# Kernel tuning notes

Measured on AMD Instinct MI355X. Metric: run time of the kernel, lower is better.

The kernel has to match this reference:

```python
import jax, jax.numpy as jnp
import numpy as np

CHAN = 24
INNER = 64
GROUPS = 8
M = 5
LAM = 1e-4
MAX_ITER = 25
BETA = 1.0
EPS = 1e-5
B, HH, WW = 128, 32, 32


def conv2d(x, w, b=None):
    # NCHW, OIHW, 3x3 SAME conv (padding = kernel//2)
    y = jax.lax.conv_general_dilated(x, w, (1, 1), 'SAME',
                                     dimension_numbers=('NCHW', 'OIHW', 'NCHW'))
    if b is not None:
        y = y + b[None, :, None, None]
    return y


def group_norm(x, g, b):
    bsz, c, h, w = x.shape
    xg = x.reshape(bsz, GROUPS, c // GROUPS, h, w)
    mu = xg.mean(axis=(2, 3, 4), keepdims=True)
    var = xg.var(axis=(2, 3, 4), keepdims=True)
    xn = ((xg - mu) / jnp.sqrt(var + EPS)).reshape(bsz, c, h, w)
    return xn * g[None, :, None, None] + b[None, :, None, None]


def batch_norm(x, g, b):
    # training-mode batch statistics over (N, H, W)
    mu = x.mean(axis=(0, 2, 3), keepdims=True)
    var = x.var(axis=(0, 2, 3), keepdims=True)
    return (x - mu) / jnp.sqrt(var + EPS) * g[None, :, None, None] + b[None, :, None, None]


def resnet_f(p, z, x):
    c1w, g1g, g1b, c2w, g2g, g2b, g3g, g3b = p
    y = group_norm(jax.nn.relu(conv2d(z, c1w)), g1g, g1b)
    return group_norm(jax.nn.relu(z + group_norm(x + conv2d(y, c2w), g2g, g2b)), g3g, g3b)


def anderson(f, x0):
    # Anderson acceleration, fixed MAX_ITER iterations (no host-sync tol break).
    bsz = x0.shape[0]
    d = x0.size // bsz
    X = jnp.zeros((bsz, M, d), x0.dtype)
    Fm = jnp.zeros((bsz, M, d), x0.dtype)
    f0 = f(x0).reshape(bsz, -1)
    X = X.at[:, 0].set(x0.reshape(bsz, -1))
    Fm = Fm.at[:, 0].set(f0)
    X = X.at[:, 1].set(f0)
    Fm = Fm.at[:, 1].set(f(f0.reshape(x0.shape)).reshape(bsz, -1))
    for k in range(2, MAX_ITER):
        n = min(k, M)
        G = Fm[:, :n] - X[:, :n]                       # [b, n, d]
        Hm = jnp.zeros((bsz, n + 1, n + 1), x0.dtype)
        Hm = Hm.at[:, 0, 1:].set(1.0).at[:, 1:, 0].set(1.0)
        Hm = Hm.at[:, 1:, 1:].set(jnp.einsum('bnd,bmd->bnm', G, G)
                                  + LAM * jnp.eye(n, dtype=x0.dtype)[None])
        yv = jnp.zeros((bsz, n + 1, 1), x0.dtype).at[:, 0, 0].set(1.0)
        alpha = jnp.linalg.solve(Hm, yv)[:, 1:, 0]     # [b, n]
        xnew = (BETA * jnp.einsum('bn,bnd->bd', alpha, Fm[:, :n])
                + (1.0 - BETA) * jnp.einsum('bn,bnd->bd', alpha, X[:, :n]))
        X = X.at[:, k % M].set(xnew)
        Fm = Fm.at[:, k % M].set(f(xnew.reshape(x0.shape)).reshape(bsz, -1))
    return X[:, (MAX_ITER - 1) % M].reshape(x0.shape)


def setup_inputs() -> dict:
    key = jax.random.key(0)
    ks = jax.random.split(key, 8)
    inp = {
        'x': jax.random.normal(ks[0], (B, 3, HH, WW), jnp.float32),
        'pre_conv_w': jax.random.normal(ks[1], (CHAN, 3, 3, 3), jnp.float32) * 0.1,
        'pre_conv_b': jnp.zeros((CHAN,), jnp.float32),
        'pre_bn_g': jnp.ones((CHAN,), jnp.float32),
        'pre_bn_b': jnp.zeros((CHAN,), jnp.float32),
        'f_conv1_w': jax.random.normal(ks[2], (INNER, CHAN, 3, 3), jnp.float32) * 0.01,
        'gn1_g': jnp.ones((INNER,), jnp.float32),
        'gn1_b': jnp.zeros((INNER,), jnp.float32),
        'f_conv2_w': jax.random.normal(ks[3], (CHAN, INNER, 3, 3), jnp.float32) * 0.01,
        'gn2_g': jnp.ones((CHAN,), jnp.float32),
        'gn2_b': jnp.zeros((CHAN,), jnp.float32),
        'gn3_g': jnp.ones((CHAN,), jnp.float32),
        'gn3_b': jnp.zeros((CHAN,), jnp.float32),
        'post_bn_g': jnp.ones((CHAN,), jnp.float32),
        'post_bn_b': jnp.zeros((CHAN,), jnp.float32),
        'fc_w': jax.random.normal(ks[4], (10, CHAN * 4 * 4), jnp.float32) * 0.05,
        'fc_b': jnp.zeros((10,), jnp.float32),
    }
    return inp


def reference(x, pre_conv_w, pre_conv_b, pre_bn_g, pre_bn_b,
              f_conv1_w, gn1_g, gn1_b, f_conv2_w, gn2_g, gn2_b, gn3_g, gn3_b,
              post_bn_g, post_bn_b, fc_w, fc_b):
    # pre: conv + BatchNorm
    xp = batch_norm(conv2d(x, pre_conv_w, pre_conv_b), pre_bn_g, pre_bn_b)
    p = (f_conv1_w, gn1_g, gn1_b, f_conv2_w, gn2_g, gn2_b, gn3_g, gn3_b)
    # DEQ fixed-point solve (eval path: train=False returns the fixed point)
    z_star = anderson(lambda z: resnet_f(p, z, xp), jnp.zeros_like(xp))
    z = resnet_f(p, z_star, xp)
    # post: relu -> BN -> avgpool(8,8) -> flatten -> linear
    h = batch_norm(jax.nn.relu(z), post_bn_g, post_bn_b)
    bsz, c, hh, ww = h.shape
    pooled = h.reshape(bsz, c, hh // 8, 8, ww // 8, 8).mean(axis=(3, 5))  # [B,C,4,4]
    return pooled.reshape(bsz, -1) @ fc_w.T + fc_b
```

## Files before the change

kernel.cpp:

```cpp
#include <hip/hip_runtime.h>
#include <hip/hip_bf16.h>

typedef __hip_bfloat16 bf16;
typedef unsigned short ushortT;
typedef __attribute__((ext_vector_type(8))) short short8;
typedef __attribute__((ext_vector_type(4))) float f32x4;

#define BB 128
#define CHAN 24
#define INNER 64
#define HW 1024
#define DD (CHAN*HW)

constexpr size_t cBD = (size_t)BB*DD;
constexpr size_t cYB = (size_t)BB*INNER*HW;

__device__ __attribute__((aligned(16))) ushortT g_xp[cBD];
__device__ __attribute__((aligned(16))) ushortT g_X[5*cBD];
__device__ __attribute__((aligned(16))) ushortT g_F[5*cBD];
__device__ __attribute__((aligned(16))) ushortT g_G[5*cBD];
__device__ __attribute__((aligned(16))) ushortT g_yb[cYB];
__device__ __attribute__((aligned(16))) ushortT g_tb[cBD];
__device__ __attribute__((aligned(16))) ushortT g_w1m[9*64*32];
__device__ __attribute__((aligned(16))) ushortT g_w2m[9*24*64];
__device__ __attribute__((aligned(16))) float g_stats2a[48];
__device__ __attribute__((aligned(16))) float g_stats2b[48];
__device__ __attribute__((aligned(16))) float g_gn1sum[BB*8*2];
__device__ __attribute__((aligned(16))) float g_gn2sum[BB*24*2];
__device__ __attribute__((aligned(16))) float g_gram[BB*25];
__device__ __attribute__((aligned(16))) float g_params[5120];
__device__ unsigned g_isbf16;

#define P_PCW 0
#define P_PCB 648
#define P_PBG 672
#define P_PBB 696
#define P_G1G 720
#define P_G1B 784
#define P_G2G 848
#define P_G2B 872
#define P_G3G 896
#define P_G3B 920
#define P_POG 944
#define P_POB 968
#define P_FCW 992
#define P_FCB 4832

__device__ __forceinline__ size_t aidx(int b, int icv, int pix){
  return (((size_t)b*3 + icv)*1024 + (size_t)pix)*8;
}
__device__ __forceinline__ float rdin(const void* p, int i){
  if (g_isbf16) return __bfloat162float(((const bf16*)p)[i]);
  return ((const float*)p)[i];
}
__device__ __forceinline__ float b2f(ushortT u){
  unsigned v = ((unsigned)u) << 16;
  return __builtin_bit_cast(float, v);
}
__device__ __forceinline__ ushortT f2b(float f){
  unsigned u = __builtin_bit_cast(unsigned, f);
  u += 0x7FFFu + ((u >> 16) & 1u);
  return (ushortT)(u >> 16);
}
__device__ __forceinline__ void ld24c(const ushortT* base, int b, int pix, float* o){
  #pragma unroll
  for (int icv=0;icv<3;icv++){
    short8 v = *(const short8*)&base[aidx(b,icv,pix)];
    #pragma unroll
    for (int j=0;j<8;j++) o[icv*8+j] = b2f((ushortT)v[j]);
  }
}
__device__ __forceinline__ void st24c(ushortT* base, int b, int pix, const float* i){
  #pragma unroll
  for (int icv=0;icv<3;icv++){
    short8 v;
    #pragma unroll
    for (int j=0;j<8;j++) v[j] = (short)f2b(i[icv*8+j]);
    *(short8*)&base[aidx(b,icv,pix)] = v;
  }
}

__global__ void detect_k(const void* g1g){
  if (threadIdx.x==0 && blockIdx.x==0){
    unsigned u = *(const unsigned*)g1g;
    g_isbf16 = (u == 0x3F803F80u) ? 1u : 0u;
  }
}

__global__ void cvt_params_k(const void* pcw, const void* pcb, const void* pbg, const void* pbb,
                             const void* g1g, const void* g1b, const void* g2g, const void* g2b,
                             const void* g3g, const void* g3b, const void* pog, const void* pob,
                             const void* fcw, const void* fcb){
  int t = threadIdx.x;
  for (int i=t;i<648;i+=256)  g_params[P_PCW+i]=rdin(pcw,i);
  for (int i=t;i<24;i+=256) { g_params[P_PCB+i]=rdin(pcb,i);
                              g_params[P_PBG+i]=rdin(pbg,i);
                              g_params[P_PBB+i]=rdin(pbb,i);
                              g_params[P_G2G+i]=rdin(g2g,i);
                              g_params[P_G2B+i]=rdin(g2b,i);
                              g_params[P_G3G+i]=rdin(g3g,i);
                              g_params[P_G3B+i]=rdin(g3b,i);
                              g_params[P_POG+i]=rdin(pog,i);
                              g_params[P_POB+i]=rdin(pob,i); }
  for (int i=t;i<64;i+=256) { g_params[P_G1G+i]=rdin(g1g,i);
                              g_params[P_G1B+i]=rdin(g1b,i); }
  for (int i=t;i<3840;i+=256) g_params[P_FCW+i]=rdin(fcw,i);
  for (int i=t;i<10;i+=256)   g_params[P_FCB+i]=rdin(fcb,i);
  for (int i=t;i<48;i+=256) { g_stats2a[i]=0.f; g_stats2b[i]=0.f; }
}

__global__ void wtm_k(const void* w1, const void* w2){
  int t = blockIdx.x*256 + threadIdx.x;
  if (t < 9*64*32){
    int ic = t & 31, oc = (t>>5)&63, s9 = t>>11;
    float v = (ic<24) ? rdin(w1, (oc*24+ic)*9 + s9) : 0.f;
    g_w1m[t] = f2b(v);
  }
  int u = t - 9*64*32;
  if (u >= 0 && u < 9*24*64){
    int ic = u & 63; int rest = u >> 6; int oc = rest % 24; int s9 = rest / 24;
    g_w2m[u] = f2b(rdin(w2, (oc*64+ic)*9 + s9));
  }
}

__global__ void zero0_k(){
  size_t base = ((size_t)blockIdx.x*256 + threadIdx.x)*8;
  short8 z = {0,0,0,0,0,0,0,0};
  *(short8*)&g_yb[base] = z;
  if (blockIdx.x < 1536) *(short8*)&g_X[base] = z;
  int t = blockIdx.x*256 + threadIdx.x;
  if (blockIdx.x < 8)  g_gn1sum[t] = 0.f;
  if (blockIdx.x < 24) g_gn2sum[t] = 0.f;
}

__global__ void preconv_k(const void* __restrict__ x){
  __shared__ float sR2d[4*48];
  int id = blockIdx.x*256 + threadIdx.x;
  int b = id >> 10, pix = id & 1023;
  int yy = pix >> 5, xx = pix & 31;
  float acc[24];
  #pragma unroll
  for (int oc=0;oc<24;oc++) acc[oc] = g_params[P_PCB+oc];
  for (int ic=0; ic<3; ic++)
    for (int ky=0; ky<3; ky++){
      int gy = yy+ky-1; if (gy<0||gy>=32) continue;
      for (int kx=0;kx<3;kx++){
        int gx = xx+kx-1; if (gx<0||gx>=32) continue;
        float v = rdin(x, ((b*3+ic)*32+gy)*32+gx);
        #pragma unroll
        for (int oc=0;oc<24;oc++)
          acc[oc] += v * g_params[P_PCW+(oc*3+ic)*9+ky*3+kx];
      }
    }
  st24c(g_tb, b, pix, acc);
  int lane = threadIdx.x & 63, wv = threadIdx.x >> 6;
  #pragma unroll
  for (int c=0;c<24;c++){
    float r = acc[c], q = acc[c]*acc[c];
    #pragma unroll
    for (int off=32;off;off>>=1){ r += __shfl_down(r,off,64); q += __shfl_down(q,off,64); }
    if (lane==0){ sR2d[wv*48+c*2]=r; sR2d[wv*48+c*2+1]=q; }
  }
  __syncthreads();
  if (threadIdx.x < 48)
    atomicAdd(&g_stats2a[threadIdx.x],
      sR2d[threadIdx.x] + sR2d[48+threadIdx.x] + sR2d[96+threadIdx.x] + sR2d[144+threadIdx.x]);
}

__global__ void bn_apply_k(){
  int id = blockIdx.x*256+threadIdx.x;
  int b = id >> 10, pix = id & 1023;
  const float inv = 1.f/(BB*HW);
  float tv[24], ov[24];
  ld24c(g_tb, b, pix, tv);
  #pragma unroll
  for (int c=0;c<24;c++){
    float mean = g_stats2a[c*2]*inv;
    float var = fmaxf(g_stats2a[c*2+1]*inv - mean*mean, 0.f);
    float rstd = rsqrtf(var + 1e-5f);
    ov[c] = (tv[c]-mean)*rstd*g_params[P_PBG+c] + g_params[P_PBB+c];
  }
  st24c(g_xp, b, pix, ov);
}

__launch_bounds__(256, 2)
__global__ void conv1_k(int s){
  __shared__ ushortT sMem[29312];
  ushortT* sA = sMem;
  ushortT* sW = sMem + 10880;
  const int tid = threadIdx.x;
  const int lane = tid & 63, wv = tid >> 6;
  const int mLane = lane & 15, q = lane >> 4;
  const int b = blockIdx.x >> 2, yt = blockIdx.x & 3;
  const ushortT* __restrict__ Xs = g_X + (size_t)s*cBD;
  if (blockIdx.x < 24) g_gn2sum[blockIdx.x*256 + tid] = 0.f;
  for (int i = tid; i < 1360; i += 256){
    int icv = i & 3, apix = i >> 2;
    int yl = apix / 34, xl = apix - yl*34;
    int gy = yt*8 - 1 + yl, gx = xl - 1;
    short8 v = {0,0,0,0,0,0,0,0};
    if (gy >= 0 && gy < 32 && gx >= 0 && gx < 32 && icv < 3)
      v = *(const short8*)&Xs[aidx(b, icv, gy*32 + gx)];
    *(short8*)&sA[(size_t)(apix*4 + (icv ^ (apix&3)))*8] = v;
  }
  for (int i = tid; i < 2304; i += 256){
    int icv = i & 3, rest = i >> 2;
    int oc = rest & 63, s9 = rest >> 6;
    short8 v = *(const short8*)&g_w1m[(size_t)((s9*64 + oc)*32) + icv*8];
    *(short8*)&sW[(size_t)((s9*64+oc)*4 + (icv ^ (oc&3)))*8] = v;
  }
  __syncthreads();
  f32x4 acc[4][4];
  #pragma unroll
  for (int mt=0;mt<4;mt++)
    #pragma unroll
    for (int nt=0;nt<4;nt++) acc[mt][nt] = (f32x4){0.f,0.f,0.f,0.f};
  for (int s9=0; s9<9; s9++){
    int ky = s9/3, kx = s9 - ky*3;
    short8 bfr[4];
    #pragma unroll
    for (int nt=0;nt<4;nt++){
      int oc = nt*16 + mLane;
      bfr[nt] = *(const short8*)&sW[(size_t)((s9*64+oc)*4 + (q ^ (oc&3)))*8];
    }
    #pragma unroll
    for (int mt=0;mt<4;mt++){
      int g = wv*4+mt;
      int apix = ((g>>1) + ky)*34 + (g&1)*16 + mLane + kx;
      short8 afr = *(const short8*)&sA[(size_t)(apix*4 + (q ^ (apix&3)))*8];
      #pragma unroll
      for (int nt=0;nt<4;nt++)
        acc[mt][nt] = __builtin_amdgcn_mfma_f32_16x16x32_bf16(afr, bfr[nt], acc[mt][nt], 0,0,0);
    }
  }
  __syncthreads();
  ushortT* sOut = sMem;
  #pragma unroll
  for (int mt=0;mt<4;mt++){
    int g = wv*4+mt;
    #pragma unroll
    for (int nt=0;nt<4;nt++){
      int oc = nt*16 + mLane;
      #pragma unroll
      for (int r=0;r<4;r++){
        int pix = (g>>1)*32 + (g&1)*16 + q*4 + r;
        sOut[pix*64 + oc] = f2b(fmaxf(acc[mt][nt][r], 0.f));
      }
    }
  }
  __syncthreads();
  float s0=0.f, s1=0.f;
  size_t gbase = ((size_t)b*1024 + yt*256)*64;
  for (int c = tid; c < 2048; c += 256){
    short8 v = *(const short8*)&sOut[c*8];
    *(short8*)&g_yb[gbase + (size_t)c*8] = v;
    #pragma unroll
    for (int j=0;j<8;j++){ float f = b2f((ushortT)v[j]); s0 += f; s1 += f*f; }
  }
  s0 += __shfl_down(s0,32); s1 += __shfl_down(s1,32);
  s0 += __shfl_down(s0,16); s1 += __shfl_down(s1,16);
  s0 += __shfl_down(s0, 8); s1 += __shfl_down(s1, 8);
  if (lane < 8){
    atomicAdd(&g_gn1sum[(b*8+lane)*2],   s0);
    atomicAdd(&g_gn1sum[(b*8+lane)*2+1], s1);
  }
}

__launch_bounds__(256, 2)
__global__ void conv2_k(){
  __shared__ ushortT sMem[35584];
  __shared__ float sAff[128];
  ushortT* sA = sMem;
  ushortT* sW = sMem + 21760;
  const int tid = threadIdx.x;
  const int lane = tid & 63, wv = tid >> 6;
  const int mLane = lane & 15, q = lane >> 4;
  const int b = blockIdx.x >> 2, yt = blockIdx.x & 3;
  if (tid < 64){
    int c = tid, gr = c>>3;
    float S = g_gn1sum[(b*8+gr)*2], Q = g_gn1sum[(b*8+gr)*2+1];
    float mean = S*(1.f/8192.f);
    float var = fmaxf(Q*(1.f/8192.f) - mean*mean, 0.f);
    float rstd = rsqrtf(var + 1e-5f);
    float sc = rstd*g_params[P_G1G+c];
    sAff[c] = sc; sAff[64+c] = g_params[P_G1B+c] - mean*sc;
  }
  __syncthreads();
  for (int i = tid; i < 2720; i += 256){
    int icv = i & 7, apix = i >> 3;
    int yl = apix / 34, xl = apix - yl*34;
    int gy = yt*8 - 1 + yl, gx = xl - 1;
    short8 v = {0,0,0,0,0,0,0,0};
    if (gy >= 0 && gy < 32 && gx >= 0 && gx < 32){
      short8 raw = *(const short8*)&g_yb[((size_t)b*1024 + gy*32+gx)*64 + icv*8];
      #pragma unroll
      for (int j=0;j<8;j++){
        int c = icv*8+j;
        v[j] = (short)f2b(b2f((ushortT)raw[j])*sAff[c] + sAff[64+c]);
      }
    }
    *(short8*)&sA[(size_t)(apix*8 + (icv ^ (apix&7)))*8] = v;
  }
  for (int i = tid; i < 1728; i += 256){
    int icv = i & 7, rest = i >> 3;
    int oc = rest % 24, s9 = rest / 24;
    short8 v = *(const short8*)&g_w2m[(size_t)((s9*24+oc)*64) + icv*8];
    *(short8*)&sW[(size_t)((s9*24+oc)*8 + (icv ^ (oc&7)))*8] = v;
  }
  __syncthreads();
  f32x4 acc[4][2];
  #pragma unroll
  for (int mt=0;mt<4;mt++){ acc[mt][0]=(f32x4){0.f,0.f,0.f,0.f}; acc[mt][1]=(f32x4){0.f,0.f,0.f,0.f}; }
  const bool nt1ok = (mLane < 8);
  for (int s9=0; s9<9; s9++){
    int ky = s9/3, kx = s9 - ky*3;
    #pragma unroll
    for (int ks=0; ks<2; ks++){
      int ib = ks*4;
      short8 bfr[2];
      { int oc = mLane;
        bfr[0] = *(const short8*)&sW[(size_t)((s9*24+oc)*8 + ((ib+q) ^ (oc&7)))*8]; }
      if (nt1ok){
        int oc = 16 + mLane;
        bfr[1] = *(const short8*)&sW[(size_t)((s9*24+oc)*8 + ((ib+q) ^ (oc&7)))*8];
      } else bfr[1] = (short8){0,0,0,0,0,0,0,0};
      #pragma unroll
      for (int mt=0;mt<4;mt++){
        int g = wv*4+mt;
        int apix = ((g>>1) + ky)*34 + (g&1)*16 + mLane + kx;
        short8 afr = *(const short8*)&sA[(size_t)(apix*8 + ((ib+q) ^ (apix&7)))*8];
        acc[mt][0] = __builtin_amdgcn_mfma_f32_16x16x32_bf16(afr, bfr[0], acc[mt][0], 0,0,0);
        acc[mt][1] = __builtin_amdgcn_mfma_f32_16x16x32_bf16(afr, bfr[1], acc[mt][1], 0,0,0);
      }
    }
  }
  #pragma unroll
  for (int nt=0;nt<2;nt++){
    int oc = nt*16 + mLane;
    bool ok = (oc < 24);
    int icv = oc >> 3, e = oc & 7;
    float s0=0.f, s1=0.f;
    if (ok){
      #pragma unroll
      for (int mt=0;mt<4;mt++){
        int g = wv*4+mt;
        #pragma unroll
        for (int r=0;r<4;r++){
          int pix = (yt*8 + (g>>1))*32 + (g&1)*16 + q*4 + r;
          size_t o = aidx(b, icv, pix) + e;
          float v = acc[mt][nt][r] + b2f(g_xp[o]);
          g_tb[o] = f2b(v);
          s0 += v; s1 += v*v;
        }
      }
    }
    s0 += __shfl_down(s0,32); s1 += __shfl_down(s1,32);
    s0 += __shfl_down(s0,16); s1 += __shfl_down(s1,16);
    if (lane < 16 && ok){
      atomicAdd(&g_gn2sum[(b*24+oc)*2],   s0);
      atomicAdd(&g_gn2sum[(b*24+oc)*2+1], s1);
    }
  }
}

template<int N>
__device__ __forceinline__ void chol_alpha(const float Kf[5][5], float* alpha){
  double K[N][N];
  #pragma unroll
  for (int i=0;i<N;i++)
    #pragma unroll
    for (int j=0;j<N;j++)
      K[i][j] = (double)Kf[i][j] + (i==j ? 1e-4 : 0.0);
  #pragma unroll
  for (int c=0;c<N;c++){
    double d = K[c][c];
    #pragma unroll
    for (int k2=0;k2<c;k2++) d -= K[c][k2]*K[c][k2];
    d = sqrt(fmax(d, 1e-300));
    K[c][c] = d;
    double inv = 1.0/d;
    #pragma unroll
    for (int r=c+1;r<N;r++){
      double v = K[r][c];
      #pragma unroll
      for (int k2=0;k2<c;k2++) v -= K[r][k2]*K[c][k2];
      K[r][c] = v*inv;
    }
  }
  double y[N];
  #pragma unroll
  for (int i=0;i<N;i++){
    double v = 1.0;
    #pragma unroll
    for (int j=0;j<i;j++) v -= K[i][j]*y[j];
    y[i] = v / K[i][i];
  }
  double w[N];
  #pragma unroll
  for (int i=N-1;i>=0;i--){
    double v = y[i];
    #pragma unroll
    for (int j=i+1;j<N;j++) v -= K[j][i]*w[j];
    w[i] = v / K[i][i];
  }
  double sum = 0.0;
  #pragma unroll
  for (int i=0;i<N;i++) sum += w[i];
  double invs = 1.0/sum;
  #pragma unroll
  for (int i=0;i<N;i++) alpha[i] = (float)(w[i]*invs);
}

__launch_bounds__(1024)
__global__ void fuse_k(int s, int n, int snext){
  __shared__ float sM2[8], sR2[8], sM3[8], sR3[8];
  __shared__ float sSc2[24], sSb2[24], sSc3[24], sSb3[24];
  __shared__ float sRed[16*16];
  __shared__ float sRedG[16*5];
  __shared__ float sAlpha[5];
  __shared__ float sStat[16*48];
  const int b = blockIdx.x;
  const int t = threadIdx.x;
  const int lane = t & 63, wv = t >> 6;
  if (t < 16) g_gn1sum[b*16 + t] = 0.f;
  if (t < 8){
    float S = g_gn2sum[(b*24+t*3)*2]   + g_gn2sum[(b*24+t*3+1)*2]   + g_gn2sum[(b*24+t*3+2)*2];
    float Q = g_gn2sum[(b*24+t*3)*2+1] + g_gn2sum[(b*24+t*3+1)*2+1] + g_gn2sum[(b*24+t*3+2)*2+1];
    float m = S*(1.f/3072.f);
    sM2[t] = m;
    sR2[t] = rsqrtf(fmaxf(Q*(1.f/3072.f) - m*m, 0.f) + 1e-5f);
  }
  __syncthreads();
  if (t < 24){
    int g = t/3;
    float sc = sR2[g]*g_params[P_G2G+t];
    sSc2[t] = sc; sSb2[t] = g_params[P_G2B+t] - sM2[g]*sc;
  }
  __syncthreads();
  float xv[24], v[24];
  ld24c(g_tb, b, t, v);
  ld24c(g_X + (size_t)s*cBD, b, t, xv);
  float p0[8], p1[8];
  #pragma unroll
  for (int g=0;g<8;g++){ p0[g]=0.f; p1[g]=0.f; }
  #pragma unroll
  for (int c=0;c<24;c++){
    float val = fmaxf(xv[c] + v[c]*sSc2[c] + sSb2[c], 0.f);
    v[c] = val;
    int g = c/3;
    p0[g] += val; p1[g] += val*val;
  }
  #pragma unroll
  for (int g=0;g<8;g++){
    #pragma unroll
    for (int off=32;off;off>>=1){ p0[g]+=__shfl_down(p0[g],off,64); p1[g]+=__shfl_down(p1[g],off,64); }
  }
  if (lane==0){
    #pragma unroll
    for (int g=0;g<8;g++){ sRed[wv*16+g*2]=p0[g]; sRed[wv*16+g*2+1]=p1[g]; }
  }
  __syncthreads();
  if (t < 8){
    float S=0.f, Q=0.f;
    #pragma unroll
    for (int w=0;w<16;w++){ S += sRed[w*16+t*2]; Q += sRed[w*16+t*2+1]; }
    float m = S*(1.f/3072.f);
    sM3[t] = m;
    sR3[t] = rsqrtf(fmaxf(Q*(1.f/3072.f) - m*m, 0.f) + 1e-5f);
  }
  __syncthreads();
  if (t < 24){
    int g = t/3;
    float sc = sR3[g]*g_params[P_G3G+t];
    sSc3[t] = sc; sSb3[t] = g_params[P_G3B+t] - sM3[g]*sc;
  }
  __syncthreads();
  float fv[24];
  #pragma unroll
  for (int c=0;c<24;c++) fv[c] = v[c]*sSc3[c] + sSb3[c];
  st24c(g_F + (size_t)s*cBD, b, t, fv);

  if (n > 0){
    float gl[24];
    #pragma unroll
    for (int c=0;c<24;c++) gl[c] = b2f(f2b(fv[c] - xv[c]));
    st24c(g_G + (size_t)s*cBD, b, t, gl);
    float part[5];
    #pragma unroll
    for (int j=0;j<5;j++) part[j] = 0.f;
    #pragma unroll
    for (int j=0;j<5;j++){
      if (j >= n) continue;
      float acc = 0.f;
      if (j == s){
        #pragma unroll
        for (int c=0;c<24;c++) acc += gl[c]*gl[c];
      } else {
        float gv[24];
        ld24c(g_G + (size_t)j*cBD, b, t, gv);
        #pragma unroll
        for (int c=0;c<24;c++) acc += gl[c]*gv[c];
      }
      part[j] = acc;
    }
    #pragma unroll
    for (int j=0;j<5;j++){
      float vv = part[j];
      #pragma unroll
      for (int off=32;off;off>>=1) vv += __shfl_down(vv,off,64);
      if (lane==0) sRedG[wv*5+j] = vv;
    }
    __syncthreads();
    if (t == 0){
      for (int j=0;j<n;j++){
        float vv = 0.f;
        for (int w=0;w<16;w++) vv += sRedG[w*5+j];
        g_gram[b*25+s*5+j] = vv;
        g_gram[b*25+j*5+s] = vv;
      }
      float Kf[5][5];
      for (int i=0;i<n;i++)
        for (int j=0;j<n;j++) Kf[i][j] = g_gram[b*25+i*5+j];
      float al[5];
      if (n==1) al[0]=1.f;
      else if (n==2) chol_alpha<2>(Kf, al);
      else if (n==3) chol_alpha<3>(Kf, al);
      else if (n==4) chol_alpha<4>(Kf, al);
      else chol_alpha<5>(Kf, al);
      for (int j=0;j<n;j++) sAlpha[j] = al[j];
    }
    __syncthreads();
    float acc[24];
    #pragma unroll
    for (int c=0;c<24;c++) acc[c] = 0.f;
    #pragma unroll
    for (int j=0;j<5;j++){
      if (j >= n) continue;
      float aj = sAlpha[j];
      if (j == s){
        #pragma unroll
        for (int c=0;c<24;c++) acc[c] += aj*b2f(f2b(fv[c]));
      } else {
        float tv2[24];
        ld24c(g_F + (size_t)j*cBD, b, t, tv2);
        #pragma unroll
        for (int c=0;c<24;c++) acc[c] += aj*tv2[c];
      }
    }
    st24c(g_X + (size_t)snext*cBD, b, t, acc);
  } else {
    #pragma unroll
    for (int c=0;c<24;c++){
      float r = fmaxf(b2f(f2b(fv[c])), 0.f);
      float q = r*r;
      #pragma unroll
      for (int off=32;off;off>>=1){ r += __shfl_down(r,off,64); q += __shfl_down(q,off,64); }
      if (lane==0){ sStat[wv*48+c*2]=r; sStat[wv*48+c*2+1]=q; }
    }
    __syncthreads();
    if (t < 48){
      float vv = 0.f;
      #pragma unroll
      for (int w=0;w<16;w++) vv += sStat[w*48+t];
      atomicAdd(&g_stats2b[t], vv);
    }
  }
}

__global__ void postfc_k(void* __restrict__ out){
  __shared__ float sPool[384];
  __shared__ float sMean[24], sRstd[24];
  int b = blockIdx.x, t = threadIdx.x;
  if (t < 24){
    const float inv = 1.f/(BB*HW);
    float mean = g_stats2b[t*2]*inv;
    float var = fmaxf(g_stats2b[t*2+1]*inv - mean*mean, 0.f);
    sMean[t] = mean; sRstd[t] = rsqrtf(var + 1e-5f);
  }
  __syncthreads();
  const ushortT* z = g_F + 4*cBD;
  for (int i=t; i<384; i+=256){
    int c = i>>4, bin = i&15, ph = bin>>2, pw = bin&3;
    int icv = c>>3, e = c&7;
    float gg = g_params[P_POG+c], bv = g_params[P_POB+c];
    float mean = sMean[c], rstd = sRstd[c];
    float sum = 0.f;
    for (int dy=0;dy<8;dy++)
      for (int dx=0;dx<8;dx++){
        int pix = (ph*8+dy)*32 + pw*8+dx;
        float vv = fmaxf(b2f(z[aidx(b,icv,pix) + e]), 0.f);
        sum += (vv-mean)*rstd*gg + bv;
      }
    sPool[i] = sum*(1.f/64.f);
  }
  __syncthreads();
  if (t < 10){
    float s2 = g_params[P_FCB+t];
    for (int k2=0;k2<384;k2++) s2 += sPool[k2]*g_params[P_FCW+t*384+k2];
    if (g_isbf16) ((bf16*)out)[b*10+t] = __float2bfloat16(s2);
    else ((float*)out)[b*10+t] = s2;
  }
}

extern "C" void kernel_launch(void* const* d_in, const int* in_sizes, int n_in,
                              void* d_out, int out_size, void* d_ws, size_t ws_size,
                              hipStream_t stream){
  const void* x   = d_in[0];
  const void* pcw = d_in[1];
  const void* pcb = d_in[2];
  const void* pbg = d_in[3];
  const void* pbb = d_in[4];
  const void* w1  = d_in[5];
  const void* g1g = d_in[6];
  const void* g1b = d_in[7];
  const void* w2  = d_in[8];
  const void* g2g = d_in[9];
  const void* g2b = d_in[10];
  const void* g3g = d_in[11];
  const void* g3b = d_in[12];
  const void* pog = d_in[13];
  const void* pob = d_in[14];
  const void* fcw = d_in[15];
  const void* fcb = d_in[16];
  (void)d_ws; (void)ws_size; (void)in_sizes; (void)n_in; (void)out_size;

  detect_k<<<1,64,0,stream>>>(g1g);
  cvt_params_k<<<1,256,0,stream>>>(pcw,pcb,pbg,pbb,g1g,g1b,g2g,g2b,g3g,g3b,pog,pob,fcw,fcb);
  wtm_k<<<126,256,0,stream>>>(w1, w2);

  preconv_k<<<512,256,0,stream>>>(x);
  bn_apply_k<<<512,256,0,stream>>>();

  zero0_k<<<4096,256,0,stream>>>();
  conv2_k<<<512,256,0,stream>>>();
  fuse_k<<<128,1024,0,stream>>>(0, 1, 1);

  for (int k=1;k<25;k++){
    int s = k%5;
    conv1_k<<<512,256,0,stream>>>(s);
    conv2_k<<<512,256,0,stream>>>();
    if (k < 24){
      int n = (k+1 < 5) ? (k+1) : 5;
      fuse_k<<<128,1024,0,stream>>>(s, n, (k+1)%5);
    } else {
      fuse_k<<<128,1024,0,stream>>>(s, 0, -1);
    }
  }

  postfc_k<<<128,256,0,stream>>>(d_out);
}
```

Baseline: 1.452 ms.

## Split fuse kernel into two 512-block passes and fold Anderson mixing into conv1

```diff
diff --git a/kernel.cpp b/kernel.cpp
--- a/kernel.cpp
+++ b/kernel.cpp
@@ -4,6 +4,7 @@
 typedef __hip_bfloat16 bf16;
 typedef unsigned short ushortT;
 typedef __attribute__((ext_vector_type(8))) short short8;
+typedef __attribute__((ext_vector_type(4))) short s16x4;
 typedef __attribute__((ext_vector_type(4))) float f32x4;
 
 #define BB 128
@@ -16,7 +17,7 @@
 constexpr size_t cYB = (size_t)BB*INNER*HW;
 
 __device__ __attribute__((aligned(16))) ushortT g_xp[cBD];
-__device__ __attribute__((aligned(16))) ushortT g_X[5*cBD];
+__device__ __attribute__((aligned(16))) ushortT g_xcur[cBD];
 __device__ __attribute__((aligned(16))) ushortT g_F[5*cBD];
 __device__ __attribute__((aligned(16))) ushortT g_G[5*cBD];
 __device__ __attribute__((aligned(16))) ushortT g_yb[cYB];
@@ -27,6 +28,8 @@
 __device__ __attribute__((aligned(16))) float g_stats2b[48];
 __device__ __attribute__((aligned(16))) float g_gn1sum[BB*8*2];
 __device__ __attribute__((aligned(16))) float g_gn2sum[BB*24*2];
+__device__ __attribute__((aligned(16))) float g_gn3p[BB*4*16];
+__device__ __attribute__((aligned(16))) float g_gramp[BB*4*5*5];
 __device__ __attribute__((aligned(16))) float g_gram[BB*25];
 __device__ __attribute__((aligned(16))) float g_params[5120];
 __device__ unsigned g_isbf16;
@@ -48,6 +51,9 @@
 
 __device__ __forceinline__ size_t aidx(int b, int icv, int pix){
   return (((size_t)b*3 + icv)*1024 + (size_t)pix)*8;
+}
+__device__ __forceinline__ size_t tidx(int b, int g, int c, int p){
+  return ((((size_t)b*64 + g)*24 + c)<<4) + p;
 }
 __device__ __forceinline__ float rdin(const void* p, int i){
   if (g_isbf16) return __bfloat162float(((const bf16*)p)[i]);
@@ -127,10 +133,9 @@
   size_t base = ((size_t)blockIdx.x*256 + threadIdx.x)*8;
   short8 z = {0,0,0,0,0,0,0,0};
   *(short8*)&g_yb[base] = z;
-  if (blockIdx.x < 1536) *(short8*)&g_X[base] = z;
-  int t = blockIdx.x*256 + threadIdx.x;
-  if (blockIdx.x < 8)  g_gn1sum[t] = 0.f;
-  if (blockIdx.x < 24) g_gn2sum[t] = 0.f;
+  if (blockIdx.x < 1536) *(short8*)&g_xcur[base] = z;
+  if (blockIdx.x < 8)  g_gn1sum[blockIdx.x*256 + threadIdx.x] = 0.f;
+  if (blockIdx.x >= 8 && blockIdx.x < 32) g_gn2sum[(blockIdx.x-8)*256 + threadIdx.x] = 0.f;
 }
 
 __global__ void preconv_k(const void* __restrict__ x){
@@ -171,36 +176,122 @@
   int id = blockIdx.x*256+threadIdx.x;
   int b = id >> 10, pix = id & 1023;
   const float inv = 1.f/(BB*HW);
-  float tv[24], ov[24];
+  float tv[24];
   ld24c(g_tb, b, pix, tv);
+  int g = pix >> 4, p = pix & 15;
   #pragma unroll
   for (int c=0;c<24;c++){
     float mean = g_stats2a[c*2]*inv;
     float var = fmaxf(g_stats2a[c*2+1]*inv - mean*mean, 0.f);
     float rstd = rsqrtf(var + 1e-5f);
-    ov[c] = (tv[c]-mean)*rstd*g_params[P_PBG+c] + g_params[P_PBB+c];
-  }
-  st24c(g_xp, b, pix, ov);
+    float ov = (tv[c]-mean)*rstd*g_params[P_PBG+c] + g_params[P_PBB+c];
+    g_xp[tidx(b,g,c,p)] = f2b(ov);
+  }
+}
+
+template<int N>
+__device__ __forceinline__ void chol_alpha(const float Kf[5][5], float* alpha){
+  double K[N][N];
+  #pragma unroll
+  for (int i=0;i<N;i++)
+    #pragma unroll
+    for (int j=0;j<N;j++)
+      K[i][j] = (double)Kf[i][j] + (i==j ? 1e-4 : 0.0);
+  #pragma unroll
+  for (int c=0;c<N;c++){
+    double d = K[c][c];
+    #pragma unroll
+    for (int k2=0;k2<c;k2++) d -= K[c][k2]*K[c][k2];
+    d = sqrt(fmax(d, 1e-300));
+    K[c][c] = d;
+    double inv = 1.0/d;
+    #pragma unroll
+    for (int r=c+1;r<N;r++){
+      double v = K[r][c];
+      #pragma unroll
+      for (int k2=0;k2<c;k2++) v -= K[r][k2]*K[c][k2];
+      K[r][c] = v*inv;
+    }
+  }
+  double y[N];
+  #pragma unroll
+  for (int i=0;i<N;i++){
+    double v = 1.0;
+    #pragma unroll
+    for (int j=0;j<i;j++) v -= K[i][j]*y[j];
+    y[i] = v / K[i][i];
+  }
+  double w[N];
+  #pragma unroll
+  for (int i=N-1;i>=0;i--){
+    double v = y[i];
+    #pragma unroll
+    for (int j=i+1;j<N;j++) v -= K[j][i]*w[j];
+    w[i] = v / K[i][i];
+  }
+  double sum = 0.0;
+  #pragma unroll
+  for (int i=0;i<N;i++) sum += w[i];
+  double invs = 1.0/sum;
+  #pragma unroll
+  for (int i=0;i<N;i++) alpha[i] = (float)(w[i]*invs);
 }
 
 __launch_bounds__(256, 2)
-__global__ void conv1_k(int s){
+__global__ void conv1_k(int na, int rA){
   __shared__ ushortT sMem[29312];
+  __shared__ float sAlpha[5];
   ushortT* sA = sMem;
   ushortT* sW = sMem + 10880;
   const int tid = threadIdx.x;
   const int lane = tid & 63, wv = tid >> 6;
   const int mLane = lane & 15, q = lane >> 4;
   const int b = blockIdx.x >> 2, yt = blockIdx.x & 3;
-  const ushortT* __restrict__ Xs = g_X + (size_t)s*cBD;
   if (blockIdx.x < 24) g_gn2sum[blockIdx.x*256 + tid] = 0.f;
+  if (tid == 0){
+    float Kf[5][5];
+    for (int i=0;i<na;i++)
+      for (int j=0;j<na;j++) Kf[i][j] = g_gram[b*25 + i*5 + j];
+    for (int j=0;j<na;j++){
+      float v = g_gramp[((b*4+0)*5 + rA)*5 + j] + g_gramp[((b*4+1)*5 + rA)*5 + j]
+              + g_gramp[((b*4+2)*5 + rA)*5 + j] + g_gramp[((b*4+3)*5 + rA)*5 + j];
+      Kf[rA][j] = v; Kf[j][rA] = v;
+    }
+    if (yt == 0)
+      for (int j=0;j<na;j++){ g_gram[b*25+rA*5+j]=Kf[rA][j]; g_gram[b*25+j*5+rA]=Kf[rA][j]; }
+    float al[5];
+    if (na==1) al[0]=1.f;
+    else if (na==2) chol_alpha<2>(Kf, al);
+    else if (na==3) chol_alpha<3>(Kf, al);
+    else if (na==4) chol_alpha<4>(Kf, al);
+    else chol_alpha<5>(Kf, al);
+    for (int j=0;j<na;j++) sAlpha[j] = al[j];
+  }
+  __syncthreads();
+  float al[5];
+  #pragma unroll
+  for (int j=0;j<5;j++) al[j] = (j<na) ? sAlpha[j] : 0.f;
   for (int i = tid; i < 1360; i += 256){
     int icv = i & 3, apix = i >> 2;
     int yl = apix / 34, xl = apix - yl*34;
     int gy = yt*8 - 1 + yl, gx = xl - 1;
     short8 v = {0,0,0,0,0,0,0,0};
-    if (gy >= 0 && gy < 32 && gx >= 0 && gx < 32 && icv < 3)
-      v = *(const short8*)&Xs[aidx(b, icv, gy*32 + gx)];
+    if (gy >= 0 && gy < 32 && gx >= 0 && gx < 32 && icv < 3){
+      int pix = gy*32 + gx;
+      float acc[8] = {0.f,0.f,0.f,0.f,0.f,0.f,0.f,0.f};
+      #pragma unroll
+      for (int j=0;j<5;j++){
+        if (j < na){
+          short8 f = *(const short8*)&g_F[(size_t)j*cBD + aidx(b,icv,pix)];
+          #pragma unroll
+          for (int e=0;e<8;e++) acc[e] += al[j]*b2f((ushortT)f[e]);
+        }
+      }
+      #pragma unroll
+      for (int e=0;e<8;e++) v[e] = (short)f2b(acc[e]);
+      if (yl >= 1 && yl < 9 && xl >= 1 && xl < 33)
+        *(short8*)&g_xcur[aidx(b,icv,pix)] = v;
+    }
     *(short8*)&sA[(size_t)(apix*4 + (icv ^ (apix&3)))*8] = v;
   }
   for (int i = tid; i < 2304; i += 256){
@@ -344,11 +435,13 @@
       #pragma unroll
       for (int mt=0;mt<4;mt++){
         int g = wv*4+mt;
+        int grp = (yt*8 + (g>>1))*2 + (g&1);
+        s16x4 xpv = *(const s16x4*)&g_xp[tidx(b, grp, oc, q*4)];
         #pragma unroll
         for (int r=0;r<4;r++){
           int pix = (yt*8 + (g>>1))*32 + (g&1)*16 + q*4 + r;
           size_t o = aidx(b, icv, pix) + e;
-          float v = acc[mt][nt][r] + b2f(g_xp[o]);
+          float v = acc[mt][nt][r] + b2f((ushortT)xpv[r]);
           g_tb[o] = f2b(v);
           s0 += v; s1 += v*v;
         }
@@ -363,66 +456,13 @@
   }
 }
 
-template<int N>
-__device__ __forceinline__ void chol_alpha(const float Kf[5][5], float* alpha){
-  double K[N][N];
-  #pragma unroll
-  for (int i=0;i<N;i++)
-    #pragma unroll
-    for (int j=0;j<N;j++)
-      K[i][j] = (double)Kf[i][j] + (i==j ? 1e-4 : 0.0);
-  #pragma unroll
-  for (int c=0;c<N;c++){
-    double d = K[c][c];
-    #pragma unroll
-    for (int k2=0;k2<c;k2++) d -= K[c][k2]*K[c][k2];
-    d = sqrt(fmax(d, 1e-300));
-    K[c][c] = d;
-    double inv = 1.0/d;
-    #pragma unroll
-    for (int r=c+1;r<N;r++){
-      double v = K[r][c];
-      #pragma unroll
-      for (int k2=0;k2<c;k2++) v -= K[r][k2]*K[c][k2];
-      K[r][c] = v*inv;
-    }
-  }
-  double y[N];
-  #pragma unroll
-  for (int i=0;i<N;i++){
-    double v = 1.0;
-    #pragma unroll
-    for (int j=0;j<i;j++) v -= K[i][j]*y[j];
-    y[i] = v / K[i][i];
-  }
-  double w[N];
-  #pragma unroll
-  for (int i=N-1;i>=0;i--){
-    double v = y[i];
-    #pragma unroll
-    for (int j=i+1;j<N;j++) v -= K[j][i]*w[j];
-    w[i] = v / K[i][i];
-  }
-  double sum = 0.0;
-  #pragma unroll
-  for (int i=0;i<N;i++) sum += w[i];
-  double invs = 1.0/sum;
-  #pragma unroll
-  for (int i=0;i<N;i++) alpha[i] = (float)(w[i]*invs);
-}
-
-__launch_bounds__(1024)
-__global__ void fuse_k(int s, int n, int snext){
-  __shared__ float sM2[8], sR2[8], sM3[8], sR3[8];
-  __shared__ float sSc2[24], sSb2[24], sSc3[24], sSb3[24];
-  __shared__ float sRed[16*16];
-  __shared__ float sRedG[16*5];
-  __shared__ float sAlpha[5];
-  __shared__ float sStat[16*48];
-  const int b = blockIdx.x;
+__launch_bounds__(256)
+__global__ void fuse_a_k(){
+  __shared__ float sM2[8], sR2[8], sSc2[24], sSb2[24];
+  __shared__ float sRed[64];
+  const int b = blockIdx.x>>2, seg = blockIdx.x&3;
   const int t = threadIdx.x;
-  const int lane = t & 63, wv = t >> 6;
-  if (t < 16) g_gn1sum[b*16 + t] = 0.f;
+  if (seg == 0 && t < 16) g_gn1sum[b*16 + t] = 0.f;
   if (t < 8){
     float S = g_gn2sum[(b*24+t*3)*2]   + g_gn2sum[(b*24+t*3+1)*2]   + g_gn2sum[(b*24+t*3+2)*2];
     float Q = g_gn2sum[(b*24+t*3)*2+1] + g_gn2sum[(b*24+t*3+1)*2+1] + g_gn2sum[(b*24+t*3+2)*2+1];
@@ -437,133 +477,124 @@
     sSc2[t] = sc; sSb2[t] = g_params[P_G2B+t] - sM2[g]*sc;
   }
   __syncthreads();
-  float xv[24], v[24];
-  ld24c(g_tb, b, t, v);
-  ld24c(g_X + (size_t)s*cBD, b, t, xv);
+  const int pix = seg*256 + t;
+  float tv[24], xv[24];
+  ld24c(g_tb, b, pix, tv);
+  ld24c(g_xcur, b, pix, xv);
   float p0[8], p1[8];
   #pragma unroll
   for (int g=0;g<8;g++){ p0[g]=0.f; p1[g]=0.f; }
   #pragma unroll
   for (int c=0;c<24;c++){
-    float val = fmaxf(xv[c] + v[c]*sSc2[c] + sSb2[c], 0.f);
-    v[c] = val;
     int g = c/3;
-    p0[g] += val; p1[g] += val*val;
+    float v = fmaxf(xv[c] + tv[c]*sSc2[c] + sSb2[c], 0.f);
+    p0[g] += v; p1[g] += v*v;
   }
   #pragma unroll
   for (int g=0;g<8;g++){
-    #pragma unroll
-    for (int off=32;off;off>>=1){ p0[g]+=__shfl_down(p0[g],off,64); p1[g]+=__shfl_down(p1[g],off,64); }
-  }
+    for (int off=32;off>0;off>>=1){ p0[g]+=__shfl_down(p0[g],off,64); p1[g]+=__shfl_down(p1[g],off,64); }
+  }
+  int lane = t&63, wv = t>>6;
   if (lane==0){
     #pragma unroll
     for (int g=0;g<8;g++){ sRed[wv*16+g*2]=p0[g]; sRed[wv*16+g*2+1]=p1[g]; }
   }
   __syncthreads();
+  if (t < 16){
+    g_gn3p[(b*4+seg)*16 + t] = sRed[t]+sRed[16+t]+sRed[32+t]+sRed[48+t];
+  }
+}
+
+__launch_bounds__(256)
+__global__ void fuse_b_k(int s, int nv){
+  __shared__ float sM2[8], sR2[8], sM3[8], sR3[8];
+  __shared__ float sSc2[24], sSb2[24], sSc3[24], sSb3[24];
+  __shared__ float sRedG[4][5];
+  __shared__ float sR2d[4*48];
+  const int b = blockIdx.x>>2, seg = blockIdx.x&3;
+  const int t = threadIdx.x;
   if (t < 8){
-    float S=0.f, Q=0.f;
-    #pragma unroll
-    for (int w=0;w<16;w++){ S += sRed[w*16+t*2]; Q += sRed[w*16+t*2+1]; }
+    float S = g_gn2sum[(b*24+t*3)*2]   + g_gn2sum[(b*24+t*3+1)*2]   + g_gn2sum[(b*24+t*3+2)*2];
+    float Q = g_gn2sum[(b*24+t*3)*2+1] + g_gn2sum[(b*24+t*3+1)*2+1] + g_gn2sum[(b*24+t*3+2)*2+1];
     float m = S*(1.f/3072.f);
-    sM3[t] = m;
-    sR3[t] = rsqrtf(fmaxf(Q*(1.f/3072.f) - m*m, 0.f) + 1e-5f);
+    sM2[t] = m;
+    sR2[t] = rsqrtf(fmaxf(Q*(1.f/3072.f) - m*m, 0.f) + 1e-5f);
+    float S3 = g_gn3p[(b*4+0)*16+t*2]   + g_gn3p[(b*4+1)*16+t*2]
+             + g_gn3p[(b*4+2)*16+t*2]   + g_gn3p[(b*4+3)*16+t*2];
+    float Q3 = g_gn3p[(b*4+0)*16+t*2+1] + g_gn3p[(b*4+1)*16+t*2+1]
+             + g_gn3p[(b*4+2)*16+t*2+1] + g_gn3p[(b*4+3)*16+t*2+1];
+    float m3 = S3*(1.f/3072.f);
+    sM3[t] = m3;
+    sR3[t] = rsqrtf(fmaxf(Q3*(1.f/3072.f) - m3*m3, 0.f) + 1e-5f);
   }
   __syncthreads();
   if (t < 24){
     int g = t/3;
-    float sc = sR3[g]*g_params[P_G3G+t];
-    sSc3[t] = sc; sSb3[t] = g_params[P_G3B+t] - sM3[g]*sc;
-  }
-  __syncthreads();
-  float fv[24];
-  #pragma unroll
-  for (int c=0;c<24;c++) fv[c] = v[c]*sSc3[c] + sSb3[c];
-  st24c(g_F + (size_t)s*cBD, b, t, fv);
-
-  if (n > 0){
-    float gl[24];
-    #pragma unroll
-    for (int c=0;c<24;c++) gl[c] = b2f(f2b(fv[c] - xv[c]));
-    st24c(g_G + (size_t)s*cBD, b, t, gl);
-    float part[5];
-    #pragma unroll
-    for (int j=0;j<5;j++) part[j] = 0.f;
-    #pragma unroll
-    for (int j=0;j<5;j++){
-      if (j >= n) continue;
-      float acc = 0.f;
-      if (j == s){
-        #pragma unroll
-        for (int c=0;c<24;c++) acc += gl[c]*gl[c];
-      } else {
-        float gv[24];
-        ld24c(g_G + (size_t)j*cBD, b, t, gv);
-        #pragma unroll
-        for (int c=0;c<24;c++) acc += gl[c]*gv[c];
-      }
-      part[j] = acc;
-    }
-    #pragma unroll
-    for (int j=0;j<5;j++){
-      float vv = part[j];
-      #pragma unroll
-      for (int off=32;off;off>>=1) vv += __shfl_down(vv,off,64);
-      if (lane==0) sRedG[wv*5+j] = vv;
-    }
-    __syncthreads();
-    if (t == 0){
-      for (int j=0;j<n;j++){
-        float vv = 0.f;
-        for (int w=0;w<16;w++) vv += sRedG[w*5+j];
-        g_gram[b*25+s*5+j] = vv;
-        g_gram[b*25+j*5+s] = vv;
-      }
-      float Kf[5][5];
-      for (int i=0;i<n;i++)
-        for (int j=0;j<n;j++) Kf[i][j] = g_gram[b*25+i*5+j];
-      float al[5];
-      if (n==1) al[0]=1.f;
-      else if (n==2) chol_alpha<2>(Kf, al);
-      else if (n==3) chol_alpha<3>(Kf, al);
-      else if (n==4) chol_alpha<4>(Kf, al);
-      else chol_alpha<5>(Kf, al);
-      for (int j=0;j<n;j++) sAlpha[j] = al[j];
-    }
-    __syncthreads();
-    float acc[24];
-    #pragma unroll
-    for (int c=0;c<24;c++) acc[c] = 0.f;
-    #pragma unroll
-    for (int j=0;j<5;j++){
-      if (j >= n) continue;
-      float aj = sAlpha[j];
-      if (j == s){
-        #pragma unroll
-        for (int c=0;c<24;c++) acc[c] += aj*b2f(f2b(fv[c]));
-      } else {
-        float tv2[24];
-        ld24c(g_F + (size_t)j*cBD, b, t, tv2);
-        #pragma unroll
-        for (int c=0;c<24;c++) acc[c] += aj*tv2[c];
-      }
-    }
-    st24c(g_X + (size_t)snext*cBD, b, t, acc);
-  } else {
+    float sc2 = sR2[g]*g_params[P_G2G+t];
+    sSc2[t] = sc2; sSb2[t] = g_params[P_G2B+t] - sM2[g]*sc2;
+    float sc3 = sR3[g]*g_params[P_G3G+t];
+    sSc3[t] = sc3; sSb3[t] = g_params[P_G3B+t] - sM3[g]*sc3;
+  }
+  __syncthreads();
+  const int pix = seg*256 + t;
+  float tv[24], xv[24], fv[24];
+  ld24c(g_tb, b, pix, tv);
+  ld24c(g_xcur, b, pix, xv);
+  #pragma unroll
+  for (int c=0;c<24;c++){
+    float v = fmaxf(xv[c] + tv[c]*sSc2[c] + sSb2[c], 0.f);
+    fv[c] = v*sSc3[c] + sSb3[c];
+  }
+  st24c(g_F + (size_t)s*cBD, b, pix, fv);
+  if (nv == 0){
+    int lane = t&63, wv = t>>6;
     #pragma unroll
     for (int c=0;c<24;c++){
       float r = fmaxf(b2f(f2b(fv[c])), 0.f);
       float q = r*r;
       #pragma unroll
       for (int off=32;off;off>>=1){ r += __shfl_down(r,off,64); q += __shfl_down(q,off,64); }
-      if (lane==0){ sStat[wv*48+c*2]=r; sStat[wv*48+c*2+1]=q; }
+      if (lane==0){ sR2d[wv*48+c*2]=r; sR2d[wv*48+c*2+1]=q; }
     }
     __syncthreads();
-    if (t < 48){
-      float vv = 0.f;
-      #pragma unroll
-      for (int w=0;w<16;w++) vv += sStat[w*48+t];
-      atomicAdd(&g_stats2b[t], vv);
-    }
+    if (t < 48)
+      atomicAdd(&g_stats2b[t],
+        sR2d[t] + sR2d[48+t] + sR2d[96+t] + sR2d[144+t]);
+    return;
+  }
+  float gl[24];
+  #pragma unroll
+  for (int c=0;c<24;c++) gl[c] = b2f(f2b(fv[c] - xv[c]));
+  st24c(g_G + (size_t)s*cBD, b, pix, gl);
+  float part[5];
+  #pragma unroll
+  for (int j=0;j<5;j++) part[j]=0.f;
+  #pragma unroll
+  for (int j=0;j<5;j++){
+    if (j>=nv) continue;
+    float acc=0.f;
+    if (j==s){
+      #pragma unroll
+      for (int c=0;c<24;c++) acc += gl[c]*gl[c];
+    } else {
+      float gv[24];
+      ld24c(g_G + (size_t)j*cBD, b, pix, gv);
+      #pragma unroll
+      for (int c=0;c<24;c++) acc += gl[c]*gv[c];
+    }
+    part[j]=acc;
+  }
+  int lane = t&63, wv = t>>6;
+  #pragma unroll
+  for (int j=0;j<5;j++){
+    float v = part[j];
+    for (int off=32;off>0;off>>=1) v += __shfl_down(v,off,64);
+    if (lane==0 && j<nv) sRedG[wv][j] = v;
+  }
+  __syncthreads();
+  if (t < 5 && t < nv){
+    float v = sRedG[0][t]+sRedG[1][t]+sRedG[2][t]+sRedG[3][t];
+    g_gramp[((b*4+seg)*5 + s)*5 + t] = v;
   }
 }
 
@@ -633,17 +664,21 @@
 
   zero0_k<<<4096,256,0,stream>>>();
   conv2_k<<<512,256,0,stream>>>();
-  fuse_k<<<128,1024,0,stream>>>(0, 1, 1);
+  fuse_a_k<<<512,256,0,stream>>>();
+  fuse_b_k<<<512,256,0,stream>>>(0, 1);
 
   for (int k=1;k<25;k++){
     int s = k%5;
-    conv1_k<<<512,256,0,stream>>>(s);
+    int na = (k<5) ? k : 5;
+    int rA = (k-1)%5;
+    conv1_k<<<512,256,0,stream>>>(na, rA);
     conv2_k<<<512,256,0,stream>>>();
+    fuse_a_k<<<512,256,0,stream>>>();
     if (k < 24){
       int n = (k+1 < 5) ? (k+1) : 5;
-      fuse_k<<<128,1024,0,stream>>>(s, n, (k+1)%5);
+      fuse_b_k<<<512,256,0,stream>>>(s, n);
     } else {
-      fuse_k<<<128,1024,0,stream>>>(s, 0, -1);
+      fuse_b_k<<<512,256,0,stream>>>(s, 0);
     }
   }
 
```

New measurement: 1.526 ms. 1.05x slower.
